# Performance work log

Hardware: AMD Instinct MI355X
Metric: run time of the kernel (lower is better)

## Reference

```python
import jax, jax.numpy as jnp
import numpy as np

K = 16            # neighbors per node
NB = 8            # number_of_basis
MAX_RADIUS = 10.0
MUL_1E = 32       # multiplicity of the 1e output block
DIM_0E = 64       # 64x0e block (structurally zero: no 1o x 0e -> 0e path)
DIM_2E = 80       # 16x2e block (structurally zero: no 1o x 0e -> 2e path)


def knn_edges(coords):
    """coords [B,N,3] -> (senders, receivers) flat int32 indices of length B*N*K.
    Edge (j -> i): j is one of the K nearest neighbors of i (self excluded),
    matching torch_geometric knn_graph(loop=False, flow=source_to_target)."""
    B, N, _ = coords.shape
    n2 = jnp.sum(coords * coords, -1)                       # [B,N]
    d2 = n2[:, :, None] + n2[:, None, :] - 2.0 * jnp.einsum('bnd,bmd->bnm', coords, coords)
    d2 = d2 + jnp.eye(N, dtype=coords.dtype) * 1e10         # exclude self-loops
    _, idx = jax.lax.top_k(-d2, K)                          # [B,N,K] neighbor ids per node
    offs = (jnp.arange(B) * N)[:, None, None]
    senders = (idx + offs).reshape(-1)
    receivers = (jnp.broadcast_to(jnp.arange(N)[None, :, None], (B, N, K)) + offs).reshape(-1)
    return senders, receivers


def gaussian_soft_one_hot(x, number):
    # x in [0,1], shape [E,1] -> [E,number]
    centers = jnp.linspace(0.0, 1.0, number).astype(x.dtype)
    sigma = 1.0 / number
    g = jnp.exp(-(x - centers) ** 2 / (2.0 * sigma * sigma))
    s = jnp.sum(g, -1, keepdims=True)
    s = jnp.where(s > 0, s, jnp.ones_like(s))
    return g / s


def setup_inputs():
    key = jax.random.key(0)
    ks = jax.random.split(key, 6)
    B, N = 8, 4096
    coords = jax.random.normal(ks[0], (B, N, 3), dtype=jnp.float32) * 10.0
    atom_types = jax.random.randint(ks[1], (B, N), 0, 20)
    residue_types = jax.random.randint(ks[2], (B, N), 0, 21)
    tp_weight = jax.random.normal(ks[3], (NB, MUL_1E), dtype=jnp.float32) / np.sqrt(NB)
    atom_emb = jax.random.normal(ks[4], (20, 112), dtype=jnp.float32).at[0].set(0.0)   # padding_idx=0
    res_emb = jax.random.normal(ks[5], (21, 112), dtype=jnp.float32).at[0].set(0.0)    # padding_idx=0
    return {"coords": coords, "atom_types": atom_types, "residue_types": residue_types,
            "tp_weight": tp_weight, "atom_emb": atom_emb, "res_emb": res_emb}


def reference(coords, atom_types, residue_types, tp_weight, atom_emb, res_emb):
    B, N, _ = coords.shape
    E = B * N * K
    senders, receivers = knn_edges(coords)
    cf = coords.reshape(-1, 3)
    r = cf[senders] - cf[receivers]                           # [E,3]
    dist = jnp.linalg.norm(r, axis=-1, keepdims=True)         # [E,1]
    r_hat = r / (dist + 1e-8)
    cutoff = jnp.clip(dist / MAX_RADIUS, 0.0, 1.0)
    rb = gaussian_soft_one_hot(cutoff, NB)                    # [E,NB]
    # FullyConnectedTensorProduct(1x1o/1e, NBx0e -> ... 32x1e ...):
    feat_1e = jnp.einsum('ev,vw,em->ewm', rb, tp_weight, r_hat) / np.sqrt(3.0)  # [E,32,3]
    # scatter_mean over receivers
    num = jax.ops.segment_sum(feat_1e.reshape(E, MUL_1E * 3), receivers, num_segments=B * N)
    cnt = jax.ops.segment_sum(jnp.ones((E,), coords.dtype), receivers, num_segments=B * N)
    agg_1e = (num / jnp.maximum(cnt, 1.0)[:, None]).reshape(B, N, MUL_1E * 3)
    zeros0 = jnp.zeros((B, N, DIM_0E), coords.dtype)
    zeros2 = jnp.zeros((B, N, DIM_2E), coords.dtype)
    pos_feats = jnp.concatenate([zeros0, agg_1e, zeros2], -1)  # [B,N,240]
    node_features = jnp.concatenate([pos_feats, atom_emb[atom_types], res_emb[residue_types]], -1)
    return node_features  # [B,N,464]
```

## Files before the change

kernel.cpp:

```cpp
#include <hip/hip_runtime.h>
#include <hip/hip_bf16.h>

#define NN    4096
#define KNEI  16
#define QPW   4
#define WPB   16
#define BLOCK (WPB * 64)
#define QPB   (WPB * QPW)
#define BIGF  3.0e38f

typedef float f32x2 __attribute__((ext_vector_type(2)));

__device__ __forceinline__ int rlane(int v, int l)
{ return __builtin_amdgcn_readlane(v, l); }
__device__ __forceinline__ float rlanef(float v, int l)
{ return __int_as_float(__builtin_amdgcn_readlane(__float_as_int(v), l)); }

template<int CTRL>
__device__ __forceinline__ void amax_step(float& f, int& i)
{
    int fs = __builtin_amdgcn_update_dpp(__float_as_int(f), __float_as_int(f),
                                         CTRL, 0xF, 0xF, false);
    int is = __builtin_amdgcn_update_dpp(i, i, CTRL, 0xF, 0xF, false);
    float ff = __int_as_float(fs);
    bool gt = ff > f;
    f = gt ? ff : f;
    i = gt ? is : i;
}

__device__ __forceinline__ void wave_amax(float f, int i, float& M, int& mi)
{
    amax_step<0x111>(f, i); amax_step<0x112>(f, i); amax_step<0x114>(f, i);
    amax_step<0x118>(f, i); amax_step<0x142>(f, i); amax_step<0x143>(f, i);
    M  = rlanef(f, 63);
    mi = rlane(i, 63);
}

__device__ __forceinline__ void row_amax(float& f, int& i)
{
    amax_step<0x121>(f, i); amax_step<0x122>(f, i);
    amax_step<0x124>(f, i); amax_step<0x128>(f, i);
}

__device__ __forceinline__ float row16_sum_dpp(float v)
{
    float f = v;
#define STEPA(CTRL)                                                          \
    { int s_ = __builtin_amdgcn_update_dpp(0, __float_as_int(f),             \
               (CTRL), 0xF, 0xF, true);                                      \
      f += __int_as_float(s_); }
    STEPA(0x111) STEPA(0x112) STEPA(0x114) STEPA(0x118)
#undef STEPA
    return f;
}

__device__ __forceinline__ float bpermf(int abyte, float v)
{ return __int_as_float(__builtin_amdgcn_ds_bpermute(abyte, __float_as_int(v))); }
__device__ __forceinline__ int bpermi(int abyte, int v)
{ return __builtin_amdgcn_ds_bpermute(abyte, v); }

__device__ __forceinline__ float sel4f(float a, float b, float c, float d, int q)
{
    float lo = (q & 1) ? b : a;
    float hi = (q & 1) ? d : c;
    return (q & 2) ? hi : lo;
}
__device__ __forceinline__ int sel4i(int a, int b, int c, int d, int q)
{
    int lo = (q & 1) ? b : a;
    int hi = (q & 1) ? d : c;
    return (q & 2) ? hi : lo;
}

#define LADDER(d, b, bi, s, si)                                   \
    {  bool gtb = (d) > (b); bool gts = (d) > (s);                \
       (s)  = __builtin_amdgcn_fmed3f((d), (s), (b));             \
       (si) = gtb ? (bi) : (gts ? j : (si));                      \
       (b)  = fmaxf((b), (d));                                    \
       (bi) = gtb ? j : (bi); }

#define REPLAY(q, xq, yq, zq)                                                \
    {   int colq = rlane(col, 16 * (q));                                     \
        int csq  = rlane(cs,  16 * (q));                                     \
        int j2 = (lane << 6) | (colq ^ lane);                                \
        float4 P = pts[j2];                                                  \
        float scr = fmaf(P.x, (xq), fmaf(P.y, (yq), fmaf(P.z, (zq), P.w)));  \
        if (j2 == q0 + (q)) scr = -BIGF;                                     \
        _Pragma("unroll")                                                    \
        for (int t = 0; t < KNEI; ++t) {                                     \
            int sv = rlane(selIdx, 16 * (q) + t);                            \
            if (j2 == sv) scr = -BIGF;                                       \
        }                                                                    \
        float M1; int i1;                                                    \
        wave_amax(scr, j2, M1, i1);                                          \
        float scr2 = (j2 == i1) ? -BIGF : scr;                               \
        float M2; int i2;                                                    \
        wave_amax(scr2, j2, M2, i2);                                         \
        bool ow = (lane == 16 * (q) + (colq & 15));                          \
        if (csq == 0) { pb0 = ow ? M1 : pb0; pbi0 = ow ? i1 : pbi0;          \
                        ps0 = ow ? M2 : ps0; psi0 = ow ? i2 : psi0; }        \
        else if (csq == 1) { pb1 = ow ? M1 : pb1; pbi1 = ow ? i1 : pbi1;     \
                        ps1 = ow ? M2 : ps1; psi1 = ow ? i2 : psi1; }        \
        else if (csq == 2) { pb2 = ow ? M1 : pb2; pbi2 = ow ? i1 : pbi2;     \
                        ps2 = ow ? M2 : ps2; psi2 = ow ? i2 : psi2; }        \
        else          { pb3 = ow ? M1 : pb3; pbi3 = ow ? i1 : pbi3;          \
                        ps3 = ow ? M2 : ps3; psi3 = ow ? i2 : psi3; }        \
    }

#define PROMOTE(k, pb, pbi, ps, psi)                                         \
    {   bool pk = own && (cs == (k));                                        \
        exh = exh || (pk && ((psi) == -1));                                  \
        (pb)  = pk ? (ps)  : (pb);                                           \
        (pbi) = pk ? (psi) : (pbi);                                          \
        (ps)  = pk ? -BIGF : (ps);                                           \
        (psi) = pk ? -1    : (psi);                                          \
    }

__global__ __launch_bounds__(BLOCK, 8)
void protein_enc_kernel(const float* __restrict__ coords,
                        const int*   __restrict__ atypes,
                        const int*   __restrict__ rtypes,
                        const float* __restrict__ tpw,
                        const float* __restrict__ aemb,
                        const float* __restrict__ remb,
                        float* __restrict__ out)
{
    __shared__ float4 pts[NN];
    __shared__ float  sW[8 * 32];

    const int tid  = threadIdx.x;
    const int lane = tid & 63;
    const int wv   = tid >> 6;
    const int bpb  = NN / QPB;
    const int batch    = blockIdx.x / bpb;
    const int nodeBase = (blockIdx.x % bpb) * QPB;

    const float* cb = coords + (size_t)batch * NN * 3;

    for (int p = tid; p < NN; p += BLOCK) {
        float x = cb[3*p], y = cb[3*p+1], z = cb[3*p+2];
        pts[p] = make_float4(x, y, z, -0.5f * (x*x + y*y + z*z));
    }
    if (tid < 256) sW[tid] = tpw[tid];
    __syncthreads();

    const int q0 = nodeBase + wv * QPW;
    const float4 P0 = pts[q0],   P1 = pts[q0+1];
    const float4 P2 = pts[q0+2], P3 = pts[q0+3];
    const float x0 = P0.x, y0 = P0.y, z0 = P0.z;
    const float x1 = P1.x, y1 = P1.y, z1 = P1.z;
    const float x2 = P2.x, y2 = P2.y, z2 = P2.z;
    const float x3 = P3.x, y3 = P3.y, z3 = P3.z;

    const f32x2 qAx = {x0, x1}, qAy = {y0, y1}, qAz = {z0, z1};
    const f32x2 qBx = {x2, x3}, qBy = {y2, y3}, qBz = {z2, z3};

    float b0 = -BIGF, s0 = -BIGF, b1 = -BIGF, s1 = -BIGF;
    float b2 = -BIGF, s2 = -BIGF, b3 = -BIGF, s3 = -BIGF;
    int bi0 = -1, si0 = -1, bi1 = -1, si1 = -1;
    int bi2 = -1, si2 = -1, bi3 = -1, si3 = -1;

    #pragma unroll 4
    for (int c = 0; c < NN / 64; ++c) {
        int j = (c << 6) | (lane ^ c);
        float4 P = pts[j];
        f32x2 Px = {P.x, P.x}, Py = {P.y, P.y}, Pz = {P.z, P.z}, Pw = {P.w, P.w};
        f32x2 dA = __builtin_elementwise_fma(Px, qAx,
                   __builtin_elementwise_fma(Py, qAy,
                   __builtin_elementwise_fma(Pz, qAz, Pw)));
        f32x2 dB = __builtin_elementwise_fma(Px, qBx,
                   __builtin_elementwise_fma(Py, qBy,
                   __builtin_elementwise_fma(Pz, qBz, Pw)));
        float d0 = dA.x, d1 = dA.y, d2 = dB.x, d3 = dB.y;
        LADDER(d0, b0, bi0, s0, si0)
        LADDER(d1, b1, bi1, s1, si1)
        LADDER(d2, b2, bi2, s2, si2)
        LADDER(d3, b3, bi3, s3, si3)
    }

    if (bi0 == q0  ) { b0 = s0; bi0 = si0; s0 = -BIGF; si0 = -1; }
    if (bi1 == q0+1) { b1 = s1; bi1 = si1; s1 = -BIGF; si1 = -1; }
    if (bi2 == q0+2) { b2 = s2; bi2 = si2; s2 = -BIGF; si2 = -1; }
    if (bi3 == q0+3) { b3 = s3; bi3 = si3; s3 = -BIGF; si3 = -1; }
    if (si0 == q0  ) { s0 = -BIGF; si0 = -1; }
    if (si1 == q0+1) { s1 = -BIGF; si1 = -1; }
    if (si2 == q0+2) { s2 = -BIGF; si2 = -1; }
    if (si3 == q0+3) { s3 = -BIGF; si3 = -1; }

    const int q = lane >> 4;
    const int gt = lane & 15;
    float pb0, pb1, pb2, pb3, ps0, ps1, ps2, ps3;
    int   pbi0, pbi1, pbi2, pbi3, psi0, psi1, psi2, psi3;
    {
        const int ab = gt << 2;
#define PULL(K, PB, PS, PBI, PSI)                                            \
        {   int a = ab + ((K) << 6);                                         \
            PB  = sel4f(bpermf(a,b0),  bpermf(a,b1),  bpermf(a,b2),  bpermf(a,b3),  q); \
            PS  = sel4f(bpermf(a,s0),  bpermf(a,s1),  bpermf(a,s2),  bpermf(a,s3),  q); \
            PBI = sel4i(bpermi(a,bi0), bpermi(a,bi1), bpermi(a,bi2), bpermi(a,bi3), q); \
            PSI = sel4i(bpermi(a,si0), bpermi(a,si1), bpermi(a,si2), bpermi(a,si3), q); \
        }
        PULL(0, pb0, ps0, pbi0, psi0)
        PULL(1, pb1, ps1, pbi1, psi1)
        PULL(2, pb2, ps2, pbi2, psi2)
        PULL(3, pb3, ps3, pbi3, psi3)
#undef PULL
    }

    int selIdx = -1;
    const int myR = gt;

    #pragma unroll 1
    for (int r = 0; r < KNEI; ++r) {
        float f = pb0; int m = pbi0;
        { bool g = pb1 > f; f = g ? pb1 : f; m = g ? ((1<<12)|pbi1) : m; }
        { bool g = pb2 > f; f = g ? pb2 : f; m = g ? ((2<<12)|pbi2) : m; }
        { bool g = pb3 > f; f = g ? pb3 : f; m = g ? ((3<<12)|pbi3) : m; }
        row_amax(f, m);

        int j   = m & 4095;
        int cs  = m >> 12;
        int col = (j & 63) ^ (j >> 6);
        bool own = (myR == (col & 15));

        if (myR == r) selIdx = j;

        bool exh = false;
        PROMOTE(0, pb0, pbi0, ps0, psi0)
        PROMOTE(1, pb1, pbi1, ps1, psi1)
        PROMOTE(2, pb2, pbi2, ps2, psi2)
        PROMOTE(3, pb3, pbi3, ps3, psi3)

        unsigned long long ex = __ballot(exh);
        if (ex) {
            if ((ex >>  0) & 0xFFFFull) REPLAY(0, x0, y0, z0)
            if ((ex >> 16) & 0xFFFFull) REPLAY(1, x1, y1, z1)
            if ((ex >> 32) & 0xFFFFull) REPLAY(2, x2, y2, z2)
            if ((ex >> 48) & 0xFFFFull) REPLAY(3, x3, y3, z3)
        }
    }

    float xq = (q & 2) ? ((q & 1) ? x3 : x2) : ((q & 1) ? x1 : x0);
    float yq = (q & 2) ? ((q & 1) ? y3 : y2) : ((q & 1) ? y1 : y0);
    float zq = (q & 2) ? ((q & 1) ? z3 : z2) : ((q & 1) ? z1 : z0);

    float4 P = pts[selIdx];
    float rx = P.x - xq, ry = P.y - yq, rz = P.z - zq;
    float dist = sqrtf(rx*rx + ry*ry + rz*rz);
    float inv  = 1.0f / (dist + 1e-8f);
    float hx = rx * inv, hy = ry * inv, hz = rz * inv;
    float cu = fminf(dist / 10.0f, 1.0f);
    float gg[8], ssum = 0.0f;
    #pragma unroll
    for (int v = 0; v < 8; ++v) {
        float d = cu - (float)v * (1.0f / 7.0f);
        gg[v] = expf(d * d * -32.0f);
        ssum += gg[v];
    }
    float is = 1.0f / ssum;
    float S[24];
    #pragma unroll
    for (int v = 0; v < 8; ++v) {
        float rbv = gg[v] * is;
        S[3*v]   = rbv * hx;
        S[3*v+1] = rbv * hy;
        S[3*v+2] = rbv * hz;
    }
    #pragma unroll
    for (int t = 0; t < 24; ++t) S[t] = row16_sum_dpp(S[t]);

    float wcol[8];
    #pragma unroll
    for (int v = 0; v < 8; ++v) wcol[v] = sW[32*v + (lane & 31)];

    const float scale = 0.036084391824351613f;
    const float4 z4 = make_float4(0.f, 0.f, 0.f, 0.f);

    #pragma unroll
    for (int qq = 0; qq < QPW; ++qq) {
        const int gq = batch * NN + q0 + qq;
        float sg[24];
        #pragma unroll
        for (int t = 0; t < 24; ++t) sg[t] = rlanef(S[t], 16 * qq + 15);

        float* onode = out + (size_t)gq * 464;
        float4* o4 = (float4*)onode;
        if (lane < 16)       o4[lane] = z4;
        else if (lane < 36)  o4[lane + 24] = z4;

        if (lane < 32) {
            float a0 = 0.f, a1 = 0.f, a2 = 0.f;
            #pragma unroll
            for (int v = 0; v < 8; ++v) {
                a0 = fmaf(wcol[v], sg[3*v],   a0);
                a1 = fmaf(wcol[v], sg[3*v+1], a1);
                a2 = fmaf(wcol[v], sg[3*v+2], a2);
            }
            onode[64 + 3*lane]     = a0 * scale;
            onode[64 + 3*lane + 1] = a1 * scale;
            onode[64 + 3*lane + 2] = a2 * scale;
        }

        const int at = atypes[gq];
        const int rt = rtypes[gq];
        if (lane < 56) {
            float4 v = (lane < 28)
                ? ((const float4*)(aemb + 112*at))[lane]
                : ((const float4*)(remb + 112*rt))[lane - 28];
            o4[60 + lane] = v;
        }
    }
}

extern "C" void kernel_launch(void* const* d_in, const int* in_sizes, int n_in,
                              void* d_out, int out_size, void* d_ws, size_t ws_size,
                              hipStream_t stream)
{
    const float* coords = (const float*)d_in[0];
    const int*   at     = (const int*)  d_in[1];
    const int*   rt     = (const int*)  d_in[2];
    const float* tpw    = (const float*)d_in[3];
    const float* ae     = (const float*)d_in[4];
    const float* re     = (const float*)d_in[5];
    float* out = (float*)d_out;

    const int B = in_sizes[1] / NN;
    dim3 grid(B * (NN / QPB));
    protein_enc_kernel<<<grid, BLOCK, 0, stream>>>(coords, at, rt, tpw, ae, re, out);
}
```

Measured before the change: 85.42 us.

## Pack candidate indices into low mantissa bits of kNN scores

Encodes the 6-bit chunk index into the low mantissa bits of each distance score, so the top-2 ladder tracks only float values via fmed3/fmax and no longer keeps separate index registers. This removes the index selects in the main scan loop and halves the bpermute traffic in the pull phase. The unroll factor rises from 4 to 8. The trade-off is that the low 6 mantissa bits of each score are dropped, so near-ties may resolve differently from exact distances and neighbor order can differ.

```diff
diff --git a/kernel.cpp b/kernel.cpp
--- a/kernel.cpp
+++ b/kernel.cpp
@@ -7,7 +7,8 @@
 #define WPB   16
 #define BLOCK (WPB * 64)
 #define QPB   (WPB * QPW)
-#define BIGF  3.0e38f
+#define NEGB  -3.0e38f
+#define PACKM 0xFFFFFFC0
 
 typedef float f32x2 __attribute__((ext_vector_type(2)));
 
@@ -56,8 +57,6 @@
 
 __device__ __forceinline__ float bpermf(int abyte, float v)
 { return __int_as_float(__builtin_amdgcn_ds_bpermute(abyte, __float_as_int(v))); }
-__device__ __forceinline__ int bpermi(int abyte, int v)
-{ return __builtin_amdgcn_ds_bpermute(abyte, v); }
 
 __device__ __forceinline__ float sel4f(float a, float b, float c, float d, int q)
 {
@@ -65,55 +64,47 @@
     float hi = (q & 1) ? d : c;
     return (q & 2) ? hi : lo;
 }
-__device__ __forceinline__ int sel4i(int a, int b, int c, int d, int q)
-{
-    int lo = (q & 1) ? b : a;
-    int hi = (q & 1) ? d : c;
-    return (q & 2) ? hi : lo;
-}
-
-#define LADDER(d, b, bi, s, si)                                   \
-    {  bool gtb = (d) > (b); bool gts = (d) > (s);                \
-       (s)  = __builtin_amdgcn_fmed3f((d), (s), (b));             \
-       (si) = gtb ? (bi) : (gts ? j : (si));                      \
-       (b)  = fmaxf((b), (d));                                    \
-       (bi) = gtb ? j : (bi); }
+
+#define LADDER(dp, b, s)                                          \
+    {  (s) = __builtin_amdgcn_fmed3f((dp), (s), (b));             \
+       (b) = fmaxf((b), (dp)); }
+
+#define SELFFIX(q, b, s)                                                     \
+    {  int cb_ = __float_as_int(b) & 63;                                     \
+       if ((((cb_) << 6) | (lane ^ cb_)) == q0 + (q)) { (b) = (s); (s) = NEGB; } \
+       int cs_ = __float_as_int(s) & 63;                                     \
+       if ((((cs_) << 6) | (lane ^ cs_)) == q0 + (q)) { (s) = NEGB; } }
 
 #define REPLAY(q, xq, yq, zq)                                                \
-    {   int colq = rlane(col, 16 * (q));                                     \
-        int csq  = rlane(cs,  16 * (q));                                     \
+    {   int colq = rlane(colw, 16 * (q));                                    \
+        int kq   = rlane(kw,   16 * (q));                                    \
         int j2 = (lane << 6) | (colq ^ lane);                                \
         float4 P = pts[j2];                                                  \
         float scr = fmaf(P.x, (xq), fmaf(P.y, (yq), fmaf(P.z, (zq), P.w)));  \
-        if (j2 == q0 + (q)) scr = -BIGF;                                     \
+        float sf = __int_as_float((__float_as_int(scr) & PACKM) | lane);     \
+        if (j2 == q0 + (q)) sf = NEGB;                                       \
         _Pragma("unroll")                                                    \
         for (int t = 0; t < KNEI; ++t) {                                     \
             int sv = rlane(selIdx, 16 * (q) + t);                            \
-            if (j2 == sv) scr = -BIGF;                                       \
+            if (j2 == sv) sf = NEGB;                                         \
         }                                                                    \
         float M1; int i1;                                                    \
-        wave_amax(scr, j2, M1, i1);                                          \
-        float scr2 = (j2 == i1) ? -BIGF : scr;                               \
+        wave_amax(sf, j2, M1, i1);                                           \
+        float sf2 = (j2 == i1) ? NEGB : sf;                                  \
         float M2; int i2;                                                    \
-        wave_amax(scr2, j2, M2, i2);                                         \
+        wave_amax(sf2, j2, M2, i2);                                          \
         bool ow = (lane == 16 * (q) + (colq & 15));                          \
-        if (csq == 0) { pb0 = ow ? M1 : pb0; pbi0 = ow ? i1 : pbi0;          \
-                        ps0 = ow ? M2 : ps0; psi0 = ow ? i2 : psi0; }        \
-        else if (csq == 1) { pb1 = ow ? M1 : pb1; pbi1 = ow ? i1 : pbi1;     \
-                        ps1 = ow ? M2 : ps1; psi1 = ow ? i2 : psi1; }        \
-        else if (csq == 2) { pb2 = ow ? M1 : pb2; pbi2 = ow ? i1 : pbi2;     \
-                        ps2 = ow ? M2 : ps2; psi2 = ow ? i2 : psi2; }        \
-        else          { pb3 = ow ? M1 : pb3; pbi3 = ow ? i1 : pbi3;          \
-                        ps3 = ow ? M2 : ps3; psi3 = ow ? i2 : psi3; }        \
-    }
-
-#define PROMOTE(k, pb, pbi, ps, psi)                                         \
-    {   bool pk = own && (cs == (k));                                        \
-        exh = exh || (pk && ((psi) == -1));                                  \
-        (pb)  = pk ? (ps)  : (pb);                                           \
-        (pbi) = pk ? (psi) : (pbi);                                          \
-        (ps)  = pk ? -BIGF : (ps);                                           \
-        (psi) = pk ? -1    : (psi);                                          \
+        if (kq == 0)      { pb0 = ow ? M1 : pb0; ps0 = ow ? M2 : ps0; }      \
+        else if (kq == 1) { pb1 = ow ? M1 : pb1; ps1 = ow ? M2 : ps1; }      \
+        else if (kq == 2) { pb2 = ow ? M1 : pb2; ps2 = ow ? M2 : ps2; }      \
+        else              { pb3 = ow ? M1 : pb3; ps3 = ow ? M2 : ps3; }      \
+    }
+
+#define PROMOTE(k, pb, ps)                                                   \
+    {   bool pk = own && (kw == (k));                                        \
+        exh = exh || (pk && ((ps) == NEGB));                                 \
+        (pb) = pk ? (ps)  : (pb);                                            \
+        (ps) = pk ? NEGB : (ps);                                             \
     }
 
 __global__ __launch_bounds__(BLOCK, 8)
@@ -155,12 +146,10 @@
     const f32x2 qAx = {x0, x1}, qAy = {y0, y1}, qAz = {z0, z1};
     const f32x2 qBx = {x2, x3}, qBy = {y2, y3}, qBz = {z2, z3};
 
-    float b0 = -BIGF, s0 = -BIGF, b1 = -BIGF, s1 = -BIGF;
-    float b2 = -BIGF, s2 = -BIGF, b3 = -BIGF, s3 = -BIGF;
-    int bi0 = -1, si0 = -1, bi1 = -1, si1 = -1;
-    int bi2 = -1, si2 = -1, bi3 = -1, si3 = -1;
-
-    #pragma unroll 4
+    float b0 = NEGB, s0 = NEGB, b1 = NEGB, s1 = NEGB;
+    float b2 = NEGB, s2 = NEGB, b3 = NEGB, s3 = NEGB;
+
+    #pragma unroll 8
     for (int c = 0; c < NN / 64; ++c) {
         int j = (c << 6) | (lane ^ c);
         float4 P = pts[j];
@@ -171,65 +160,62 @@
         f32x2 dB = __builtin_elementwise_fma(Px, qBx,
                    __builtin_elementwise_fma(Py, qBy,
                    __builtin_elementwise_fma(Pz, qBz, Pw)));
-        float d0 = dA.x, d1 = dA.y, d2 = dB.x, d3 = dB.y;
-        LADDER(d0, b0, bi0, s0, si0)
-        LADDER(d1, b1, bi1, s1, si1)
-        LADDER(d2, b2, bi2, s2, si2)
-        LADDER(d3, b3, bi3, s3, si3)
-    }
-
-    if (bi0 == q0  ) { b0 = s0; bi0 = si0; s0 = -BIGF; si0 = -1; }
-    if (bi1 == q0+1) { b1 = s1; bi1 = si1; s1 = -BIGF; si1 = -1; }
-    if (bi2 == q0+2) { b2 = s2; bi2 = si2; s2 = -BIGF; si2 = -1; }
-    if (bi3 == q0+3) { b3 = s3; bi3 = si3; s3 = -BIGF; si3 = -1; }
-    if (si0 == q0  ) { s0 = -BIGF; si0 = -1; }
-    if (si1 == q0+1) { s1 = -BIGF; si1 = -1; }
-    if (si2 == q0+2) { s2 = -BIGF; si2 = -1; }
-    if (si3 == q0+3) { s3 = -BIGF; si3 = -1; }
-
-    const int q = lane >> 4;
+        float d0 = __int_as_float((__float_as_int(dA.x) & PACKM) | c);
+        float d1 = __int_as_float((__float_as_int(dA.y) & PACKM) | c);
+        float d2 = __int_as_float((__float_as_int(dB.x) & PACKM) | c);
+        float d3 = __int_as_float((__float_as_int(dB.y) & PACKM) | c);
+        LADDER(d0, b0, s0)
+        LADDER(d1, b1, s1)
+        LADDER(d2, b2, s2)
+        LADDER(d3, b3, s3)
+    }
+
+    SELFFIX(0, b0, s0)
+    SELFFIX(1, b1, s1)
+    SELFFIX(2, b2, s2)
+    SELFFIX(3, b3, s3)
+
+    const int q  = lane >> 4;
     const int gt = lane & 15;
     float pb0, pb1, pb2, pb3, ps0, ps1, ps2, ps3;
-    int   pbi0, pbi1, pbi2, pbi3, psi0, psi1, psi2, psi3;
     {
         const int ab = gt << 2;
-#define PULL(K, PB, PS, PBI, PSI)                                            \
+#define PULL(K, PB, PS)                                                      \
         {   int a = ab + ((K) << 6);                                         \
-            PB  = sel4f(bpermf(a,b0),  bpermf(a,b1),  bpermf(a,b2),  bpermf(a,b3),  q); \
-            PS  = sel4f(bpermf(a,s0),  bpermf(a,s1),  bpermf(a,s2),  bpermf(a,s3),  q); \
-            PBI = sel4i(bpermi(a,bi0), bpermi(a,bi1), bpermi(a,bi2), bpermi(a,bi3), q); \
-            PSI = sel4i(bpermi(a,si0), bpermi(a,si1), bpermi(a,si2), bpermi(a,si3), q); \
+            PB = sel4f(bpermf(a,b0), bpermf(a,b1), bpermf(a,b2), bpermf(a,b3), q); \
+            PS = sel4f(bpermf(a,s0), bpermf(a,s1), bpermf(a,s2), bpermf(a,s3), q); \
         }
-        PULL(0, pb0, ps0, pbi0, psi0)
-        PULL(1, pb1, ps1, pbi1, psi1)
-        PULL(2, pb2, ps2, pbi2, psi2)
-        PULL(3, pb3, ps3, pbi3, psi3)
+        PULL(0, pb0, ps0)
+        PULL(1, pb1, ps1)
+        PULL(2, pb2, ps2)
+        PULL(3, pb3, ps3)
 #undef PULL
     }
 
     int selIdx = -1;
-    const int myR = gt;
 
     #pragma unroll 1
     for (int r = 0; r < KNEI; ++r) {
-        float f = pb0; int m = pbi0;
-        { bool g = pb1 > f; f = g ? pb1 : f; m = g ? ((1<<12)|pbi1) : m; }
-        { bool g = pb2 > f; f = g ? pb2 : f; m = g ? ((2<<12)|pbi2) : m; }
-        { bool g = pb3 > f; f = g ? pb3 : f; m = g ? ((3<<12)|pbi3) : m; }
-        row_amax(f, m);
-
-        int j   = m & 4095;
-        int cs  = m >> 12;
-        int col = (j & 63) ^ (j >> 6);
-        bool own = (myR == (col & 15));
-
-        if (myR == r) selIdx = j;
+        float f = fmaxf(fmaxf(pb0, pb1), fmaxf(pb2, pb3));
+        int k = (f == pb3) ? 3 : ((f == pb2) ? 2 : ((f == pb1) ? 1 : 0));
+        int cw = __float_as_int(f) & 63;
+        int col = gt + (k << 4);
+        int jl = (cw << 6) | (col ^ cw);
+        int i = (k << 12) | jl;
+        row_amax(f, i);
+
+        int j  = i & 4095;
+        int kw = i >> 12;
+        int colw = (j & 63) ^ (j >> 6);
+        bool own = (gt == (colw & 15));
+
+        if (gt == r) selIdx = j;
 
         bool exh = false;
-        PROMOTE(0, pb0, pbi0, ps0, psi0)
-        PROMOTE(1, pb1, pbi1, ps1, psi1)
-        PROMOTE(2, pb2, pbi2, ps2, psi2)
-        PROMOTE(3, pb3, pbi3, ps3, psi3)
+        PROMOTE(0, pb0, ps0)
+        PROMOTE(1, pb1, ps1)
+        PROMOTE(2, pb2, ps2)
+        PROMOTE(3, pb3, ps3)
 
         unsigned long long ex = __ballot(exh);
         if (ex) {
```

Result: faster. 73.80 us (-13.6%).
